# Kernel tuning notes

Measured on AMD Instinct MI355X. Metric: run time of the kernel, lower is better.

Reference implementation:

```python
import jax, jax.numpy as jnp
import numpy as np

W = H = 64
CONFIGS = [(1, 3), (2, 3), (3, 3)]  # (dilation, kernel_size)
OUT_PER_CFG = 32
IN_CH = 32


def build_mask():
    # One (W+1, H+1) mask per config, broadcast over (out, in) channels.
    masks = []
    for d, k in CONFIGS:
        m = np.zeros((W + 1, H + 1), dtype=np.float32)
        k1 = (k - 1) * (d - 1) + k  # effective dilated kernel extent
        s1 = (W - k1) // 2 + 1
        e1 = (W + k1) // 2 + 1
        s2 = (H - k1) // 2 + 1
        e2 = (H + k1) // 2 + 1
        m[s1:e1:d, s2:e2:d] = 1.0
        masks.append(np.broadcast_to(m, (OUT_PER_CFG, 1, W + 1, H + 1)))
    return jnp.asarray(np.concatenate(masks, axis=0))  # (96, 1, 65, 65)


def setup_inputs() -> dict:
    key = jax.random.key(0)
    k1, k2 = jax.random.split(key)
    x = jax.random.normal(k1, (16, IN_CH, W, H), dtype=jnp.float32)
    # small init so tanh does not saturate
    weight = jax.random.normal(k2, (OUT_PER_CFG * len(CONFIGS), IN_CH, W + 1, H + 1), dtype=jnp.float32) * 0.01
    mask = build_mask()
    gamma = jnp.ones((OUT_PER_CFG * len(CONFIGS),), dtype=jnp.float32)
    beta = jnp.zeros((OUT_PER_CFG * len(CONFIGS),), dtype=jnp.float32)
    return {"x": x, "weight": weight, "mask": mask, "gamma": gamma, "beta": beta}


def reference(x, weight, mask, gamma, beta):
    # circular pad: last dim by H//2 each side, dim -2 by W//2 each side
    xp = jnp.pad(x, ((0, 0), (0, 0), (W // 2, W // 2), (H // 2, H // 2)), mode="wrap")
    y = jax.lax.conv_general_dilated(
        xp, weight * mask,
        window_strides=(1, 1), padding="VALID",
        dimension_numbers=("NCHW", "OIHW", "NCHW"),
    )  # (B, 96, 64, 64)
    # BatchNorm2d in training mode: batch statistics over (N, H, W), eps=1e-5
    mean = jnp.mean(y, axis=(0, 2, 3))
    var = jnp.var(y, axis=(0, 2, 3))
    yn = (y - mean[None, :, None, None]) * jax.lax.rsqrt(var + 1e-5)[None, :, None, None]
    yn = yn * gamma[None, :, None, None] + beta[None, :, None, None]
    return jnp.tanh(yn)
```

## Files before the change

### kernel.cpp

```cpp
#include <hip/hip_runtime.h>
#include <math.h>

#define BATCH 16
#define CIN 32
#define COUT 96
#define WH 64
#define IMG (WH*WH)
#define NPIX (BATCH*IMG)
#define PWELEMS (3*9*32*32)
#define XTELEMS (BATCH*IMG*CIN)
#define NBLK 768

typedef __attribute__((ext_vector_type(8))) short short8;
typedef __attribute__((ext_vector_type(4))) float floatx4;

__device__ __forceinline__ unsigned short f2bf(float f) {
    union { float f; unsigned u; } v; v.f = f;
    unsigned r = v.u + 0x7FFFu + ((v.u >> 16) & 1u);
    return (unsigned short)(r >> 16);
}
__device__ __forceinline__ float bf2f(unsigned short u) {
    union { unsigned u; float f; } v; v.u = (unsigned)u << 16; return v.f;
}

#define GLDS(src, dst) __builtin_amdgcn_global_load_lds( \
    (const __attribute__((address_space(1))) void*)(src), \
    (__attribute__((address_space(3))) void*)(dst), 16, 0, 0)

__device__ __forceinline__ float fast_tanh(float xv) {
    float e = __expf(2.0f * xv);
    return fmaf(-2.0f, __builtin_amdgcn_rcpf(e + 1.0f), 1.0f);
}

__global__ __launch_bounds__(256) void prep_kernel(
    const float* __restrict__ x, const float* __restrict__ w,
    unsigned short* __restrict__ xT, unsigned short* __restrict__ pw,
    float* __restrict__ gsum, float* __restrict__ gsq,
    unsigned* __restrict__ cnt)
{
    int blk = blockIdx.x;
    if (blk < 512) {
        int gid  = blk * 256 + threadIdx.x;
        int pt   = gid >> 1;
        int half = gid & 1;
        int b    = pt >> 12;
        int pix  = pt & 4095;
        const float* xb = x + ((size_t)b * CIN + half * 16) * IMG + pix;
        unsigned packed[8];
#pragma unroll
        for (int c2 = 0; c2 < 8; c2++) {
            unsigned short lo = f2bf(xb[(size_t)(2 * c2) * IMG]);
            unsigned short hi = f2bf(xb[(size_t)(2 * c2 + 1) * IMG]);
            packed[c2] = (unsigned)lo | ((unsigned)hi << 16);
        }
        uint4* dst = (uint4*)(xT + (size_t)pt * 32 + half * 16);
        dst[0] = make_uint4(packed[0], packed[1], packed[2], packed[3]);
        dst[1] = make_uint4(packed[4], packed[5], packed[6], packed[7]);
    } else if (blk < 620) {
        int e = (blk - 512) * 256 + threadIdx.x;
        if (e >= PWELEMS) return;
        int cfg = e / (9 * 1024);
        int rem = e % (9 * 1024);
        int tap = rem >> 10;
        int oc  = (rem >> 5) & 31;
        int c   = rem & 31;
        int d   = cfg + 1;
        int du  = tap / 3, dv = tap % 3;
        size_t idx = (((size_t)(cfg * 32 + oc) * CIN + c) * 65 + (32 + (du - 1) * d)) * 65
                     + (32 + (dv - 1) * d);
        pw[e] = f2bf(w[idx]);
    } else {
        int e = threadIdx.x;
        if (e < COUT) { gsum[e] = 0.f; gsq[e] = 0.f; }
        if (e == COUT) *cnt = 0u;
    }
}

__global__ __launch_bounds__(256, 3) void conv_bn_kernel(
    const unsigned short* __restrict__ xT, const unsigned short* __restrict__ pw,
    float* __restrict__ gsum, float* __restrict__ gsq,
    unsigned* __restrict__ cnt,
    const float* __restrict__ gamma, const float* __restrict__ beta,
    float* __restrict__ out)
{
    __shared__ __align__(16) unsigned short tile[10 * 2048];
    __shared__ float red_s[4][32];
    __shared__ float red_q[4][32];
    __shared__ float sc_a[32];
    __shared__ float sc_b[32];

    int bid  = blockIdx.x;
    int rowg = bid & 15;
    int rest = bid >> 4;
    int cfg  = rest % 3;
    int b    = rest / 3;
    int d    = cfg + 1;
    int i0   = rowg * 4;

    int t    = threadIdx.x;
    int wv   = t >> 6;
    int lane = t & 63;
    int l15  = lane & 15;
    int quad = lane >> 4;

    const unsigned short* xTb = xT + (size_t)b * IMG * 32;
#pragma unroll
    for (int rr = 0; rr < 10; rr++) {
        int gi = (i0 - 3 + rr) & 63;
        GLDS(xTb + (size_t)gi * 2048 + t * 8, &tile[rr * 2048 + t * 8]);
    }

    const unsigned short* pwc = pw + (size_t)cfg * 9 * 32 * 32;
    short8 af[2][9];
#pragma unroll
    for (int h = 0; h < 2; h++)
#pragma unroll
        for (int tap = 0; tap < 9; tap++)
            af[h][tap] = *(const short8*)(pwc + ((tap * 32 + h * 16 + l15) * 32 + quad * 8));

    __syncthreads();

    float ss[2][4], qq[2][4];
#pragma unroll
    for (int h = 0; h < 2; h++)
#pragma unroll
        for (int r = 0; r < 4; r++) { ss[h][r] = 0.f; qq[h][r] = 0.f; }

    unsigned ypk[2][4][2];
    int row = i0 + wv;

#pragma unroll
    for (int cgi = 0; cgi < 4; cgi++) {
        floatx4 a0 = {0.f, 0.f, 0.f, 0.f};
        floatx4 a1 = {0.f, 0.f, 0.f, 0.f};
#pragma unroll
        for (int du = 0; du < 3; du++) {
            int rowloc = wv + 3 + (du - 1) * d;
            const unsigned short* rbase = &tile[rowloc * 2048 + quad * 8];
#pragma unroll
            for (int dv = 0; dv < 3; dv++) {
                int col = (cgi * 16 + l15 + (dv - 1) * d) & 63;
                short8 bf = *(const short8*)(rbase + col * 32);
                a0 = __builtin_amdgcn_mfma_f32_16x16x32_bf16(af[0][du * 3 + dv], bf, a0, 0, 0, 0);
                a1 = __builtin_amdgcn_mfma_f32_16x16x32_bf16(af[1][du * 3 + dv], bf, a1, 0, 0, 0);
            }
        }
#pragma unroll
        for (int r = 0; r < 4; r++) {
            float v0 = a0[r], v1 = a1[r];
            unsigned short h0 = f2bf(v0), h1 = f2bf(v1);
            if (cgi & 1) {
                ypk[0][r][cgi >> 1] |= (unsigned)h0 << 16;
                ypk[1][r][cgi >> 1] |= (unsigned)h1 << 16;
            } else {
                ypk[0][r][cgi >> 1] = (unsigned)h0;
                ypk[1][r][cgi >> 1] = (unsigned)h1;
            }
            ss[0][r] += v0; qq[0][r] = fmaf(v0, v0, qq[0][r]);
            ss[1][r] += v1; qq[1][r] = fmaf(v1, v1, qq[1][r]);
        }
    }

#pragma unroll
    for (int h = 0; h < 2; h++)
#pragma unroll
        for (int r = 0; r < 4; r++) {
            float s = ss[h][r], q = qq[h][r];
            for (int m = 1; m < 16; m <<= 1) {
                s += __shfl_xor(s, m, 64);
                q += __shfl_xor(q, m, 64);
            }
            if (l15 == 0) {
                red_s[wv][h * 16 + quad * 4 + r] = s;
                red_q[wv][h * 16 + quad * 4 + r] = q;
            }
        }
    __syncthreads();

    if (t < 32) {
        float S = red_s[0][t] + red_s[1][t] + red_s[2][t] + red_s[3][t];
        atomicAdd(&gsum[cfg * 32 + t], S);
    } else if (t < 64) {
        int o = t - 32;
        float Q = red_q[0][o] + red_q[1][o] + red_q[2][o] + red_q[3][o];
        atomicAdd(&gsq[cfg * 32 + o], Q);
    }
    __syncthreads();

    if (t == 0) {
        __hip_atomic_fetch_add(cnt, 1u, __ATOMIC_RELAXED, __HIP_MEMORY_SCOPE_AGENT);
        while (__hip_atomic_load(cnt, __ATOMIC_RELAXED, __HIP_MEMORY_SCOPE_AGENT) < NBLK)
            __builtin_amdgcn_s_sleep(2);
    }
    __syncthreads();

    if (t < 32) {
        int ch = cfg * 32 + t;
        float S = __hip_atomic_load(&gsum[ch], __ATOMIC_RELAXED, __HIP_MEMORY_SCOPE_AGENT);
        float Q = __hip_atomic_load(&gsq[ch],  __ATOMIC_RELAXED, __HIP_MEMORY_SCOPE_AGENT);
        const float inv_n = 1.0f / (float)NPIX;
        float mean = S * inv_n;
        float var  = Q * inv_n - mean * mean;
        float a    = gamma[ch] * rsqrtf(var + 1e-5f);
        sc_a[t] = a;
        sc_b[t] = beta[ch] - mean * a;
    }
    __syncthreads();

#pragma unroll
    for (int h = 0; h < 2; h++)
#pragma unroll
        for (int r = 0; r < 4; r++) {
            int m0  = quad * 4 + r;
            int chl = h * 16 + m0;
            float a  = sc_a[chl];
            float bb = sc_b[chl];
            float* obase = out + ((size_t)b * COUT + cfg * 32 + chl) * IMG
                               + (size_t)row * WH + l15;
#pragma unroll
            for (int g = 0; g < 2; g++) {
                unsigned pk = ypk[h][r][g];
                obase[(2 * g) * 16]     = fast_tanh(fmaf(bf2f((unsigned short)(pk & 0xffffu)), a, bb));
                obase[(2 * g + 1) * 16] = fast_tanh(fmaf(bf2f((unsigned short)(pk >> 16)), a, bb));
            }
        }
}

extern "C" void kernel_launch(void* const* d_in, const int* in_sizes, int n_in,
                              void* d_out, int out_size, void* d_ws, size_t ws_size,
                              hipStream_t stream) {
    const float* x     = (const float*)d_in[0];
    const float* w     = (const float*)d_in[1];
    const float* gamma = (const float*)d_in[3];
    const float* beta  = (const float*)d_in[4];
    float* out = (float*)d_out;

    unsigned short* xT = (unsigned short*)d_ws;
    unsigned short* pw = xT + XTELEMS;
    float* gsum = (float*)(pw + PWELEMS + 32);
    float* gsq  = gsum + 128;
    unsigned* cnt = (unsigned*)(gsq + 128);

    prep_kernel<<<621, 256, 0, stream>>>(x, w, xT, pw, gsum, gsq, cnt);
    conv_bn_kernel<<<NBLK, 256, 0, stream>>>(xT, pw, gsum, gsq, cnt,
                                             gamma, beta, out);
}
```

Measured before the change: 123.2 us.

## Use hierarchical grid barrier and padded atomics to cut contention

The single global counter barrier becomes a two-level tree: blocks in groups of eight bump a per-group counter, the last arrival in each group bumps a root counter, and the last group sets per-group go-flags that each block polls. The per-channel sum and sum-of-squares accumulators and the counters are padded to 64-byte strides so they no longer share cache lines. Gamma and beta are loaded before the barrier. This is meant to reduce atomic contention and polling traffic on one hot cache line, at the cost of more workspace and one extra atomic hop for the last block in each group.

```diff
diff --git a/kernel.cpp b/kernel.cpp
--- a/kernel.cpp
+++ b/kernel.cpp
@@ -10,6 +10,9 @@
 #define PWELEMS (3*9*32*32)
 #define XTELEMS (BATCH*IMG*CIN)
 #define NBLK 768
+#define NGRP 96
+#define PAD 16
+#define ZWORDS (4*NGRP*PAD + PAD)
 
 typedef __attribute__((ext_vector_type(8))) short short8;
 typedef __attribute__((ext_vector_type(4))) float floatx4;
@@ -35,8 +38,7 @@
 __global__ __launch_bounds__(256) void prep_kernel(
     const float* __restrict__ x, const float* __restrict__ w,
     unsigned short* __restrict__ xT, unsigned short* __restrict__ pw,
-    float* __restrict__ gsum, float* __restrict__ gsq,
-    unsigned* __restrict__ cnt)
+    unsigned* __restrict__ zbase)
 {
     int blk = blockIdx.x;
     if (blk < 512) {
@@ -70,16 +72,15 @@
                      + (32 + (dv - 1) * d);
         pw[e] = f2bf(w[idx]);
     } else {
-        int e = threadIdx.x;
-        if (e < COUT) { gsum[e] = 0.f; gsq[e] = 0.f; }
-        if (e == COUT) *cnt = 0u;
+        for (int i = threadIdx.x; i < ZWORDS; i += 256) zbase[i] = 0u;
     }
 }
 
 __global__ __launch_bounds__(256, 3) void conv_bn_kernel(
     const unsigned short* __restrict__ xT, const unsigned short* __restrict__ pw,
     float* __restrict__ gsum, float* __restrict__ gsq,
-    unsigned* __restrict__ cnt,
+    unsigned* __restrict__ gcnt, unsigned* __restrict__ ggo,
+    unsigned* __restrict__ groot,
     const float* __restrict__ gamma, const float* __restrict__ beta,
     float* __restrict__ out)
 {
@@ -117,6 +118,9 @@
 #pragma unroll
         for (int tap = 0; tap < 9; tap++)
             af[h][tap] = *(const short8*)(pwc + ((tap * 32 + h * 16 + l15) * 32 + quad * 8));
+
+    float gam = 0.f, bet = 0.f;
+    if (t < 32) { gam = gamma[cfg * 32 + t]; bet = beta[cfg * 32 + t]; }
 
     __syncthreads();
 
@@ -179,31 +183,43 @@
 
     if (t < 32) {
         float S = red_s[0][t] + red_s[1][t] + red_s[2][t] + red_s[3][t];
-        atomicAdd(&gsum[cfg * 32 + t], S);
+        atomicAdd(&gsum[(cfg * 32 + t) * PAD], S);
     } else if (t < 64) {
         int o = t - 32;
         float Q = red_q[0][o] + red_q[1][o] + red_q[2][o] + red_q[3][o];
-        atomicAdd(&gsq[cfg * 32 + o], Q);
+        atomicAdd(&gsq[(cfg * 32 + o) * PAD], Q);
     }
     __syncthreads();
 
     if (t == 0) {
-        __hip_atomic_fetch_add(cnt, 1u, __ATOMIC_RELAXED, __HIP_MEMORY_SCOPE_AGENT);
-        while (__hip_atomic_load(cnt, __ATOMIC_RELAXED, __HIP_MEMORY_SCOPE_AGENT) < NBLK)
-            __builtin_amdgcn_s_sleep(2);
+        int g = bid >> 3;
+        unsigned r = __hip_atomic_fetch_add(&gcnt[g * PAD], 1u,
+                                            __ATOMIC_RELAXED, __HIP_MEMORY_SCOPE_AGENT);
+        if (r == 7u) {
+            unsigned rr = __hip_atomic_fetch_add(groot, 1u,
+                                                 __ATOMIC_RELAXED, __HIP_MEMORY_SCOPE_AGENT);
+            if (rr == (unsigned)(NGRP - 1)) {
+                for (int gg = 0; gg < NGRP; gg++)
+                    __hip_atomic_store(&ggo[gg * PAD], 1u,
+                                       __ATOMIC_RELAXED, __HIP_MEMORY_SCOPE_AGENT);
+            }
+        }
+        while (__hip_atomic_load(&ggo[g * PAD], __ATOMIC_RELAXED,
+                                 __HIP_MEMORY_SCOPE_AGENT) == 0u)
+            __builtin_amdgcn_s_sleep(4);
     }
     __syncthreads();
 
     if (t < 32) {
         int ch = cfg * 32 + t;
-        float S = __hip_atomic_load(&gsum[ch], __ATOMIC_RELAXED, __HIP_MEMORY_SCOPE_AGENT);
-        float Q = __hip_atomic_load(&gsq[ch],  __ATOMIC_RELAXED, __HIP_MEMORY_SCOPE_AGENT);
+        float S = __hip_atomic_load(&gsum[ch * PAD], __ATOMIC_RELAXED, __HIP_MEMORY_SCOPE_AGENT);
+        float Q = __hip_atomic_load(&gsq[ch * PAD],  __ATOMIC_RELAXED, __HIP_MEMORY_SCOPE_AGENT);
         const float inv_n = 1.0f / (float)NPIX;
         float mean = S * inv_n;
         float var  = Q * inv_n - mean * mean;
-        float a    = gamma[ch] * rsqrtf(var + 1e-5f);
+        float a    = gam * rsqrtf(var + 1e-5f);
         sc_a[t] = a;
-        sc_b[t] = beta[ch] - mean * a;
+        sc_b[t] = bet - mean * a;
     }
     __syncthreads();
 
@@ -238,10 +254,12 @@
     unsigned short* xT = (unsigned short*)d_ws;
     unsigned short* pw = xT + XTELEMS;
     float* gsum = (float*)(pw + PWELEMS + 32);
-    float* gsq  = gsum + 128;
-    unsigned* cnt = (unsigned*)(gsq + 128);
-
-    prep_kernel<<<621, 256, 0, stream>>>(x, w, xT, pw, gsum, gsq, cnt);
-    conv_bn_kernel<<<NBLK, 256, 0, stream>>>(xT, pw, gsum, gsq, cnt,
+    float* gsq  = gsum + NGRP * PAD;
+    unsigned* gcnt  = (unsigned*)(gsq + NGRP * PAD);
+    unsigned* ggo   = gcnt + NGRP * PAD;
+    unsigned* groot = ggo + NGRP * PAD;
+
+    prep_kernel<<<621, 256, 0, stream>>>(x, w, xT, pw, (unsigned*)gsum);
+    conv_bn_kernel<<<NBLK, 256, 0, stream>>>(xT, pw, gsum, gsq, gcnt, ggo, groot,
                                              gamma, beta, out);
 }
```

Result: faster. 116.0 us (-5.8%).
